# Kernel optimization log

Hardware: AMD Instinct MI355X
Metric: run time of the kernel (lower is better)

The kernel has to match this reference:

```python
import jax, jax.numpy as jnp
import numpy as np

B, S, C = 8, 4096, 1024
H, D, K = 16, 64, 256  # heads, per-head dim, linformer projection dim


def setup_inputs() -> dict:
    key = jax.random.key(0)
    ks = jax.random.split(key, 10)
    sc = 0.02
    return {
        "tensor": jax.random.normal(ks[0], (B, S, C), jnp.float32),
        "to_q_w": jax.random.normal(ks[1], (D, C), jnp.float32) * sc,
        "to_k_w": jax.random.normal(ks[2], (D, C), jnp.float32) * sc,
        "to_v_w": jax.random.normal(ks[3], (D, C), jnp.float32) * sc,
        "wq_w": jax.random.normal(ks[4], (H, D, D), jnp.float32) * sc,
        "wq_b": jnp.zeros((H, D), jnp.float32),
        "wk_w": jax.random.normal(ks[5], (H, D, D), jnp.float32) * sc,
        "wk_b": jnp.zeros((H, D), jnp.float32),
        "wv_w": jax.random.normal(ks[6], (H, D, D), jnp.float32) * sc,
        "wv_b": jnp.zeros((H, D), jnp.float32),
        "E_w": jax.random.normal(ks[7], (K, S), jnp.float32) * sc,
        "E_b": jnp.zeros((K,), jnp.float32),
        "F_w": jax.random.normal(ks[8], (K, S), jnp.float32) * sc,
        "F_b": jnp.zeros((K,), jnp.float32),
        "wo_w": jax.random.normal(ks[9], (C, H * D), jnp.float32) * sc,
        "wo_b": jnp.zeros((C,), jnp.float32),
    }


def reference(tensor, to_q_w, to_k_w, to_v_w, wq_w, wq_b, wk_w, wk_b,
              wv_w, wv_b, E_w, E_b, F_w, F_b, wo_w, wo_b):
    # Shared Q/K/V projections (no bias), recomputed identically per head in torch.
    Q = jnp.einsum('bsc,dc->bsd', tensor, to_q_w)   # [B,S,D]
    Kt = jnp.einsum('bsc,dc->bsd', tensor, to_k_w)
    V = jnp.einsum('bsc,dc->bsd', tensor, to_v_w)

    # Per-head linear layers w_q/w_k/w_v, vectorized over heads.
    QW = jnp.einsum('bsd,hed->bhse', Q, wq_w) + wq_b[None, :, None, :]   # [B,H,S,D]
    KW = jnp.einsum('bsd,hed->bhse', Kt, wk_w) + wk_b[None, :, None, :]  # [B,H,S,D]
    VW = jnp.einsum('bsd,hed->bhse', V, wv_w) + wv_b[None, :, None, :]   # [B,H,S,D]

    # E projection compresses the sequence axis: [B,H,S,D] -> [B,H,D,K]
    KE = jnp.einsum('bhsd,ks->bhdk', KW, E_w) + E_b  # bias broadcasts over last axis K
    # F projection for values, result kept as [B,H,K,D]
    VF = jnp.einsum('bhsd,ks->bhkd', VW, F_w) + F_b[:, None]

    scores = jnp.einsum('bhsd,bhdk->bhsk', QW, KE) / jnp.sqrt(jnp.float32(D))
    P = jax.nn.softmax(scores, axis=-1)              # [B,H,S,K]

    out_h = jnp.einsum('bhsk,bhkd->bhsd', P, VF)     # [B,H,S,D]
    # torch.cat(heads, dim=2): head-major feature layout
    out = out_h.transpose(0, 2, 1, 3).reshape(tensor.shape[0], tensor.shape[1], -1)
    out = jax.nn.gelu(out, approximate=False)        # F.gelu default is exact erf
    out = jnp.einsum('bsf,cf->bsc', out, wo_w) + wo_b
    return out
```

## Files before the change

kernel.cpp:

```cpp
#include <hip/hip_runtime.h>
#include <hip/hip_bf16.h>
#include <math.h>

constexpr int Bn = 8, Sn = 4096, Cn = 1024, Hn = 16, Dn = 64, Kn = 256;
constexpr int BS = Bn * Sn;

typedef __attribute__((ext_vector_type(8))) short bhalf8;
typedef __attribute__((ext_vector_type(4))) float floatx4;
typedef __attribute__((ext_vector_type(4))) unsigned int uix4;

__device__ __forceinline__ float gelu_erf(float x) {
    float z  = x * 0.70710678118654752f;
    float az = fabsf(z);
    float t  = __fdividef(1.0f, fmaf(0.3275911f, az, 1.0f));
    float p  = fmaf(t, 1.061405429f, -1.453152027f);
    p = fmaf(t, p, 1.421413741f);
    p = fmaf(t, p, -0.284496736f);
    p = fmaf(t, p, 0.254829592f);
    p *= t;
    float e  = exp2f(z * z * -1.4426950408889634f);
    float er = copysignf(fmaf(-p, e, 1.0f), z);
    return 0.5f * x * (1.0f + er);
}

__device__ __forceinline__ void gload16(const void* g, void* l) {
    __builtin_amdgcn_global_load_lds(
        (const __attribute__((address_space(1))) unsigned int*)g,
        (__attribute__((address_space(3))) unsigned int*)l,
        16, 0, 0);
}

__global__ __launch_bounds__(256) void k_cast(const float* __restrict__ src, __hip_bfloat16* __restrict__ dst)
{
    int i = (blockIdx.x * 256 + threadIdx.x) * 4;
    float4 v = *reinterpret_cast<const float4*>(src + i);
    union { __hip_bfloat16 h[4]; uint2 u; } pk;
    pk.h[0] = __float2bfloat16(v.x); pk.h[1] = __float2bfloat16(v.y);
    pk.h[2] = __float2bfloat16(v.z); pk.h[3] = __float2bfloat16(v.w);
    *reinterpret_cast<uint2*>(dst + i) = pk.u;
}

__global__ __launch_bounds__(256) void k_qkv(const float* __restrict__ tensor,
    const __hip_bfloat16* __restrict__ Wb,
    __hip_bfloat16* __restrict__ Qb, float* __restrict__ Kp, float* __restrict__ Vp)
{
    __shared__ __align__(16) char Al[64 * 128];
    const int t = threadIdx.x;
    const int w = t >> 6, lane = t & 63, lc = lane & 15, g = lane >> 4;
    const int m0 = blockIdx.x * 64;
    const int wm = (w >> 1) * 32, wn = (w & 1) * 96;
    const int lrow = t >> 2, lq = t & 3;

    floatx4 acc[2][6];
#pragma unroll
    for (int mt = 0; mt < 2; mt++)
#pragma unroll
        for (int nt = 0; nt < 6; nt++) acc[mt][nt] = (floatx4){0.f, 0.f, 0.f, 0.f};

    const float* arow = tensor + (size_t)(m0 + lrow) * 1024;
    float4 f[4];
#pragma unroll
    for (int j = 0; j < 4; j++) f[j] = *reinterpret_cast<const float4*>(arow + (lq + j * 4) * 4);

    for (int kc = 0; kc < 1024; kc += 64) {
        __syncthreads();
#pragma unroll
        for (int j = 0; j < 4; j++) {
            union { __hip_bfloat16 h[4]; uint2 u; } pk;
            pk.h[0] = __float2bfloat16(f[j].x);
            pk.h[1] = __float2bfloat16(f[j].y);
            pk.h[2] = __float2bfloat16(f[j].z);
            pk.h[3] = __float2bfloat16(f[j].w);
            int byt = lrow * 128 + (((lq + j * 4) * 8) ^ ((lrow & 7) << 4));
            *reinterpret_cast<uint2*>(Al + byt) = pk.u;
        }
        __syncthreads();
        int kcn = (kc + 64 < 1024) ? kc + 64 : 0;
#pragma unroll
        for (int j = 0; j < 4; j++) f[j] = *reinterpret_cast<const float4*>(arow + kcn + (lq + j * 4) * 4);
#pragma unroll
        for (int ks = 0; ks < 2; ks++) {
            bhalf8 a[2];
#pragma unroll
            for (int mt = 0; mt < 2; mt++) {
                int row = wm + mt * 16 + lc;
                a[mt] = *reinterpret_cast<const bhalf8*>(Al + row * 128 + ((ks * 64 + g * 16) ^ ((row & 7) << 4)));
            }
#pragma unroll
            for (int nt = 0; nt < 6; nt++) {
                bhalf8 bf = *reinterpret_cast<const bhalf8*>(&Wb[(size_t)(wn + nt * 16 + lc) * 1024 + kc + ks * 32 + g * 8]);
#pragma unroll
                for (int mt = 0; mt < 2; mt++)
                    acc[mt][nt] = __builtin_amdgcn_mfma_f32_16x16x32_bf16(a[mt], bf, acc[mt][nt], 0, 0, 0);
            }
        }
    }
#pragma unroll
    for (int mt = 0; mt < 2; mt++)
#pragma unroll
        for (int nt = 0; nt < 6; nt++) {
            int n = wn + nt * 16 + lc;
#pragma unroll
            for (int i = 0; i < 4; i++) {
                size_t s = (size_t)m0 + wm + mt * 16 + g * 4 + i;
                float v = acc[mt][nt][i];
                if (n < 64)       Qb[s * 64 + n] = __float2bfloat16(v);
                else if (n < 128) Kp[s * 64 + (n - 64)] = v;
                else              Vp[s * 64 + (n - 128)] = v;
            }
        }
}

__global__ __launch_bounds__(256) void k_rowsum(const float* __restrict__ E, const float* __restrict__ F,
                                                float* __restrict__ sumE, float* __restrict__ sumF)
{
    __shared__ float red[256];
    const float* src = blockIdx.y ? F : E;
    float* dst = blockIdx.y ? sumF : sumE;
    const int k = blockIdx.x;
    const int t = threadIdx.x;
    float a = 0.f;
#pragma unroll
    for (int i = 0; i < 16; i++) a += src[(size_t)k * Sn + t + i * 256];
    red[t] = a;
    __syncthreads();
    for (int s = 128; s > 0; s >>= 1) {
        if (t < s) red[t] += red[t + s];
        __syncthreads();
    }
    if (t == 0) dst[k] = red[0];
}

__global__ __launch_bounds__(256) void k_compress(const float* __restrict__ E, const float* __restrict__ F,
    const float* __restrict__ Kp, const float* __restrict__ Vp,
    float* __restrict__ Part)
{
    __shared__ float Es[64 * 33];
    __shared__ float Ps[32 * 64];
    const int zz = blockIdx.z;
    const int mat = zz >> 4, chunk = zz & 15;
    const float* A = mat ? F : E;
    const float* Bm = mat ? Vp : Kp;
    const int b = blockIdx.y;
    const int k0 = blockIdx.x * 64;
    const int sbeg = chunk * 256;
    const int t = threadIdx.x, tx = t & 15, ty = t >> 4;
    float acc[4][4] = {};
    for (int sc = sbeg; sc < sbeg + 256; sc += 32) {
#pragma unroll
        for (int ii = 0; ii < 2; ii++) {
            int idx4 = t + ii * 256;
            int row = idx4 >> 3, col4 = idx4 & 7;
            float4 v = *reinterpret_cast<const float4*>(&A[(size_t)(k0 + row) * Sn + sc + col4 * 4]);
            float* d2 = &Es[row * 33 + col4 * 4];
            d2[0] = v.x; d2[1] = v.y; d2[2] = v.z; d2[3] = v.w;
        }
#pragma unroll
        for (int ii = 0; ii < 2; ii++) {
            int idx4 = t + ii * 256;
            int row = idx4 >> 4, col4 = idx4 & 15;
            float4 v = *reinterpret_cast<const float4*>(&Bm[((size_t)b * Sn + sc + row) * Dn + col4 * 4]);
            float* d2 = &Ps[row * 64 + col4 * 4];
            d2[0] = v.x; d2[1] = v.y; d2[2] = v.z; d2[3] = v.w;
        }
        __syncthreads();
#pragma unroll 8
        for (int kk = 0; kk < 32; kk++) {
            float a[4], w[4];
#pragma unroll
            for (int i = 0; i < 4; i++) a[i] = Es[(ty * 4 + i) * 33 + kk];
#pragma unroll
            for (int j = 0; j < 4; j++) w[j] = Ps[kk * 64 + tx * 4 + j];
#pragma unroll
            for (int i = 0; i < 4; i++)
#pragma unroll
                for (int j = 0; j < 4; j++) acc[i][j] = fmaf(a[i], w[j], acc[i][j]);
        }
        __syncthreads();
    }
    float* pb = Part + (size_t)zz * 131072 + (size_t)b * 16384 + blockIdx.x * 4096;
#pragma unroll
    for (int i = 0; i < 4; i++) {
        float4 v = make_float4(acc[i][0], acc[i][1], acc[i][2], acc[i][3]);
        *reinterpret_cast<float4*>(&pb[(ty * 4 + i) * 64 + tx * 4]) = v;
    }
}

__global__ __launch_bounds__(256) void k_cred(const float* __restrict__ Part,
    __hip_bfloat16* __restrict__ Kc16, __hip_bfloat16* __restrict__ Vc16)
{
    int gid = blockIdx.x * 256 + threadIdx.x;
    int mat = gid >> 17;
    int rem = gid & 131071;
    const float* p = Part + (size_t)mat * 16 * 131072 + rem;
    float s = 0.f;
#pragma unroll
    for (int c = 0; c < 16; c++) s += p[(size_t)c * 131072];
    __hip_bfloat16* dst = mat ? Vc16 : Kc16;
    dst[rem] = __float2bfloat16(s);
}

__global__ __launch_bounds__(256) void k_headw(const float* __restrict__ wq, const float* __restrict__ wqb,
    const float* __restrict__ wk, const float* __restrict__ wkb,
    __hip_bfloat16* __restrict__ Wqk16, float* __restrict__ uArr, float* __restrict__ gArr,
    float* __restrict__ cw, float* __restrict__ cu, float* __restrict__ cg)
{
    __shared__ float wqL[64 * 64], wkL[64 * 64];
    const int h = blockIdx.x, t = threadIdx.x;
#pragma unroll
    for (int ii = 0; ii < 4; ii++) {
        int idx4 = (t + ii * 256) * 4;
        *reinterpret_cast<float4*>(&wqL[idx4]) = *reinterpret_cast<const float4*>(&wq[(size_t)h * 4096 + idx4]);
        *reinterpret_cast<float4*>(&wkL[idx4]) = *reinterpret_cast<const float4*>(&wk[(size_t)h * 4096 + idx4]);
    }
    __syncthreads();
#pragma unroll 2
    for (int ii = 0; ii < 16; ii++) {
        int idx = t + ii * 256;
        int d = idx >> 6, dp = idx & 63;
        float acc = 0.f;
        for (int e = 0; e < 64; e++) acc = fmaf(wqL[e * 64 + d], wkL[e * 64 + dp], acc);
        Wqk16[(size_t)h * 4096 + idx] = __float2bfloat16(acc);
    }
    if (t < 64) {
        int d = t;
        float au = 0.f, ag = 0.f, aw = 0.f;
        for (int e = 0; e < 64; e++) {
            float q = wqL[e * 64 + d];
            au = fmaf(q, wkb[h * 64 + e], au);
            ag += q;
            aw = fmaf(wqb[h * 64 + e], wkL[e * 64 + d], aw);
        }
        uArr[h * 64 + d] = au; gArr[h * 64 + d] = ag; cw[h * 64 + d] = aw;
    }
    if (t == 0) {
        float acu = 0.f, acg = 0.f;
        for (int e = 0; e < 64; e++) {
            acu = fmaf(wqb[h * 64 + e], wkb[h * 64 + e], acu);
            acg += wqb[h * 64 + e];
        }
        cu[h] = acu; cg[h] = acg;
    }
}

__global__ __launch_bounds__(256) void k_proj(
    const __hip_bfloat16* __restrict__ Kc16, const __hip_bfloat16* __restrict__ Vc16,
    const __hip_bfloat16* __restrict__ Wqk16, const __hip_bfloat16* __restrict__ wv16,
    const float* __restrict__ uArr, const float* __restrict__ gArr,
    const float* __restrict__ cw, const float* __restrict__ cu, const float* __restrict__ cg,
    const float* __restrict__ sumE, const float* __restrict__ Eb,
    const float* __restrict__ sumF, const float* __restrict__ Fb,
    const float* __restrict__ wvb,
    __hip_bfloat16* __restrict__ KEqT, __hip_bfloat16* __restrict__ VFT, float* __restrict__ c0)
{
    const int h = blockIdx.x, b = blockIdx.y;
    const int bh = b * Hn + h;
    const int t = threadIdx.x;
    const int w = t >> 6, lane = t & 63, lc = lane & 15, g = lane >> 4;
    const __hip_bfloat16* KcB = Kc16 + (size_t)b * (Kn * 64);
    const __hip_bfloat16* VcB = Vc16 + (size_t)b * (Kn * 64);
    const __hip_bfloat16* Wq = Wqk16 + (size_t)h * 4096;
    const __hip_bfloat16* Wv = wv16 + (size_t)h * 4096;

    {
        floatx4 acc[4][4];
#pragma unroll
        for (int mt = 0; mt < 4; mt++)
#pragma unroll
            for (int nt = 0; nt < 4; nt++) acc[mt][nt] = (floatx4){0.f, 0.f, 0.f, 0.f};
#pragma unroll
        for (int ks = 0; ks < 2; ks++) {
            bhalf8 a[4];
#pragma unroll
            for (int mt = 0; mt < 4; mt++)
                a[mt] = *reinterpret_cast<const bhalf8*>(Wq + (mt * 16 + lc) * 64 + ks * 32 + g * 8);
#pragma unroll
            for (int nt = 0; nt < 4; nt++) {
                bhalf8 bf = *reinterpret_cast<const bhalf8*>(KcB + (size_t)(w * 64 + nt * 16 + lc) * 64 + ks * 32 + g * 8);
#pragma unroll
                for (int mt = 0; mt < 4; mt++)
                    acc[mt][nt] = __builtin_amdgcn_mfma_f32_16x16x32_bf16(a[mt], bf, acc[mt][nt], 0, 0, 0);
            }
        }
#pragma unroll
        for (int mt = 0; mt < 4; mt++) {
            float4 u4 = *reinterpret_cast<const float4*>(&uArr[h * 64 + mt * 16 + g * 4]);
            float4 g4 = *reinterpret_cast<const float4*>(&gArr[h * 64 + mt * 16 + g * 4]);
#pragma unroll
            for (int nt = 0; nt < 4; nt++) {
                int k = w * 64 + nt * 16 + lc;
                float sE = sumE[k], eb = Eb[k];
                union { __hip_bfloat16 hh[4]; uint2 uu; } pk;
                pk.hh[0] = __float2bfloat16(acc[mt][nt][0] + u4.x * sE + g4.x * eb);
                pk.hh[1] = __float2bfloat16(acc[mt][nt][1] + u4.y * sE + g4.y * eb);
                pk.hh[2] = __float2bfloat16(acc[mt][nt][2] + u4.z * sE + g4.z * eb);
                pk.hh[3] = __float2bfloat16(acc[mt][nt][3] + u4.w * sE + g4.w * eb);
                *reinterpret_cast<uint2*>(&KEqT[((size_t)bh * 256 + k) * 64 + mt * 16 + g * 4]) = pk.uu;
            }
        }
    }
    {
        floatx4 acc[4][4];
#pragma unroll
        for (int mt = 0; mt < 4; mt++)
#pragma unroll
            for (int nt = 0; nt < 4; nt++) acc[mt][nt] = (floatx4){0.f, 0.f, 0.f, 0.f};
#pragma unroll
        for (int ks = 0; ks < 2; ks++) {
            bhalf8 a[4];
#pragma unroll
            for (int mt = 0; mt < 4; mt++)
                a[mt] = *reinterpret_cast<const bhalf8*>(VcB + (size_t)(w * 64 + mt * 16 + lc) * 64 + ks * 32 + g * 8);
#pragma unroll
            for (int nt = 0; nt < 4; nt++) {
                bhalf8 bf = *reinterpret_cast<const bhalf8*>(Wv + (nt * 16 + lc) * 64 + ks * 32 + g * 8);
#pragma unroll
                for (int mt = 0; mt < 4; mt++)
                    acc[mt][nt] = __builtin_amdgcn_mfma_f32_16x16x32_bf16(a[mt], bf, acc[mt][nt], 0, 0, 0);
            }
        }
#pragma unroll
        for (int mt = 0; mt < 4; mt++) {
            int kbase = w * 64 + mt * 16 + g * 4;
            float4 sF4 = *reinterpret_cast<const float4*>(&sumF[kbase]);
            float4 fb4 = *reinterpret_cast<const float4*>(&Fb[kbase]);
#pragma unroll
            for (int nt = 0; nt < 4; nt++) {
                int e = nt * 16 + lc;
                float wvbe = wvb[h * 64 + e];
                union { __hip_bfloat16 hh[4]; uint2 uu; } pk;
                pk.hh[0] = __float2bfloat16(acc[mt][nt][0] + wvbe * sF4.x + fb4.x);
                pk.hh[1] = __float2bfloat16(acc[mt][nt][1] + wvbe * sF4.y + fb4.y);
                pk.hh[2] = __float2bfloat16(acc[mt][nt][2] + wvbe * sF4.z + fb4.z);
                pk.hh[3] = __float2bfloat16(acc[mt][nt][3] + wvbe * sF4.w + fb4.w);
                *reinterpret_cast<uint2*>(&VFT[(size_t)bh * 16384 + (size_t)e * 256 + kbase]) = pk.uu;
            }
        }
    }
    {
        constexpr float SC = 0.18033688011112042f;
        const __hip_bfloat16* kr = KcB + (size_t)t * 64;
        float acc = 0.f;
#pragma unroll
        for (int dp = 0; dp < 64; dp++)
            acc = fmaf(cw[h * 64 + dp], __bfloat162float(kr[dp]), acc);
        c0[(size_t)bh * 256 + t] = (acc + cu[h] * sumE[t] + cg[h] * Eb[t]) * SC;
    }
}

__global__ __launch_bounds__(256, 2) void k_attn(
    const __hip_bfloat16* __restrict__ Qb, const __hip_bfloat16* __restrict__ KEqT,
    const float* __restrict__ c0s, const __hip_bfloat16* __restrict__ VFT,
    __hip_bfloat16* __restrict__ cat)
{
    __shared__ __align__(16) char Kl[32768];
    __shared__ __align__(16) char Vl[32768];
    __shared__ __align__(16) char Pl[4 * 2048];
    __shared__ float c0L[256];

    int fid = blockIdx.x + (blockIdx.y << 3);
    int xcd = fid & 7, local = fid >> 3;
    int bh = xcd * 16 + (local & 15);
    int chunk = local >> 4;
    const int b = bh >> 4, h = bh & 15;
    const int t = threadIdx.x;
    const int w = t >> 6, lane = t & 63, lc = lane & 15, g = lane >> 4;

    const char* Kg = reinterpret_cast<const char*>(KEqT + (size_t)bh * 16384);
#pragma unroll
    for (int it = 0; it < 8; ++it) {
        int idx = it * 256 + t;
        int row = idx >> 3, ch = idx & 7;
        gload16(Kg + row * 128 + (ch ^ (row & 7)) * 16, Kl + it * 4096 + w * 1024);
    }
    const char* Vg = reinterpret_cast<const char*>(VFT + (size_t)bh * 16384);
#pragma unroll
    for (int it = 0; it < 8; ++it) {
        int idx = it * 256 + t;
        int row = idx >> 5, c16 = idx & 31;
        gload16(Vg + row * 512 + (c16 ^ (row & 7)) * 16, Vl + it * 4096 + w * 1024);
    }
    c0L[t] = c0s[(size_t)bh * 256 + t];
    __syncthreads();

    char* Pw = Pl + w * 2048;
    const int sbase = chunk * 512 + w * 16;
    constexpr float SC = 0.18033688011112042f;

    const __hip_bfloat16* Q0 = Qb + ((size_t)b * Sn + sbase + lc) * 64 + g * 8;
    bhalf8 bq0 = *reinterpret_cast<const bhalf8*>(Q0);
    bhalf8 bq1 = *reinterpret_cast<const bhalf8*>(Q0 + 32);

    for (int tile = 0; tile < 8; ++tile) {
        asm volatile("" ::: "memory");
        const int s0 = sbase + tile * 64;

        floatx4 acc[16];
#pragma unroll
        for (int rt = 0; rt < 16; rt++) {
            int row = rt * 16 + lc;
            bhalf8 a0 = *reinterpret_cast<const bhalf8*>(Kl + row * 128 + (g ^ (row & 7)) * 16);
            bhalf8 a1 = *reinterpret_cast<const bhalf8*>(Kl + row * 128 + ((4 + g) ^ (row & 7)) * 16);
            floatx4 z = (floatx4){0.f, 0.f, 0.f, 0.f};
            z = __builtin_amdgcn_mfma_f32_16x16x32_bf16(a0, bq0, z, 0, 0, 0);
            z = __builtin_amdgcn_mfma_f32_16x16x32_bf16(a1, bq1, z, 0, 0, 0);
            acc[rt] = z;
        }

        bhalf8 nq0 = bq0, nq1 = bq1;
        if (tile < 7) {
            const __hip_bfloat16* nQ = Qb + ((size_t)b * Sn + s0 + 64 + lc) * 64 + g * 8;
            nq0 = *reinterpret_cast<const bhalf8*>(nQ);
            nq1 = *reinterpret_cast<const bhalf8*>(nQ + 32);
        }

        float ls = 0.f;
#pragma unroll
        for (int rt = 0; rt < 16; rt++) {
            float4 c4 = *reinterpret_cast<const float4*>(&c0L[rt * 16 + g * 4]);
#pragma unroll
            for (int i = 0; i < 4; i++) {
                float e = exp2f(fmaf(acc[rt][i], SC, ((const float*)&c4)[i]));
                acc[rt][i] = e;
                ls += e;
            }
        }
        ls += __shfl_xor(ls, 16);
        ls += __shfl_xor(ls, 32);
        const float linv = 1.f / ls;

        floatx4 o[4];
#pragma unroll
        for (int dt = 0; dt < 4; dt++) o[dt] = (floatx4){0.f, 0.f, 0.f, 0.f};
#pragma unroll
        for (int ph = 0; ph < 4; ++ph) {
#pragma unroll
            for (int rr = 0; rr < 4; rr++) {
                int rt = ph * 4 + rr;
                union { __hip_bfloat16 hh[4]; uint2 u; } pk;
#pragma unroll
                for (int i = 0; i < 4; i++) pk.hh[i] = __float2bfloat16(acc[rt][i]);
                int byt = lc * 128 + ((rr * 32 + g * 8) ^ ((lc & 7) << 4));
                *reinterpret_cast<uint2*>(Pw + byt) = pk.u;
            }
#pragma unroll
            for (int kk = 0; kk < 2; kk++) {
                int ks = ph * 2 + kk;
                bhalf8 pa = *reinterpret_cast<const bhalf8*>(
                    Pw + lc * 128 + ((kk * 64 + g * 16) ^ ((lc & 7) << 4)));
#pragma unroll
                for (int dt = 0; dt < 4; dt++) {
                    int e = dt * 16 + lc;
                    bhalf8 bv = *reinterpret_cast<const bhalf8*>(
                        Vl + e * 512 + (((ks * 4 + g) ^ (e & 7)) * 16));
                    o[dt] = __builtin_amdgcn_mfma_f32_16x16x32_bf16(pa, bv, o[dt], 0, 0, 0);
                }
            }
        }

#pragma unroll
        for (int i = 0; i < 4; i++) {
            float inv_i = __shfl(linv, g * 4 + i);
            int row = g * 4 + i;
#pragma unroll
            for (int dt = 0; dt < 4; dt++) {
                float x = o[dt][i] * inv_i;
                int byt = row * 128 + ((dt * 32 + lc * 2) ^ ((row >> 2) << 5));
                *reinterpret_cast<__hip_bfloat16*>(Pw + byt) = __float2bfloat16(gelu_erf(x));
            }
        }
#pragma unroll
        for (int pass = 0; pass < 2; ++pass) {
            int c = pass * 64 + lane;
            int row = c >> 3, off = (c & 7) * 16;
            uix4 v = *reinterpret_cast<const uix4*>(Pw + row * 128 + (off ^ ((row >> 2) << 5)));
            __hip_bfloat16* dst = cat + ((size_t)b * Sn + s0 + row) * 1024 + h * 64;
            __builtin_nontemporal_store(v, reinterpret_cast<uix4*>(reinterpret_cast<char*>(dst) + off));
        }

        bq0 = nq0; bq1 = nq1;
    }
}

__global__ __launch_bounds__(256, 2) void k_out(
    const __hip_bfloat16* __restrict__ cat, const __hip_bfloat16* __restrict__ wo16,
    const float* __restrict__ wob, float* __restrict__ out)
{
    __shared__ __align__(16) char As[32768];
    __shared__ __align__(16) char Bs[16384];

    const int t = threadIdx.x;
    const int w = t >> 6, lane = t & 63, lc = lane & 15, g = lane >> 4;
    int fid = blockIdx.x + (blockIdx.y << 3);
    int xcd = fid & 7, local = fid >> 3;
    int mt0 = xcd * 16 + (local >> 3);
    int nt0 = local & 7;
    const int m0 = mt0 * 256;
    const int n0 = nt0 * 128;
    const int wm = (w >> 1) * 128, wn = (w & 1) * 64;

    floatx4 acc[8][4];
#pragma unroll
    for (int mt = 0; mt < 8; mt++)
#pragma unroll
        for (int nt = 0; nt < 4; nt++) acc[mt][nt] = (floatx4){0.f, 0.f, 0.f, 0.f};

    for (int kc = 0; kc < 1024; kc += 64) {
        __syncthreads();
#pragma unroll
        for (int call = 0; call < 8; ++call) {
            int idx = call * 256 + t;
            int row = idx >> 3, ch = idx & 7;
            int sch = ch ^ (row & 7);
            gload16(cat + ((size_t)(m0 + row) * 1024 + kc + sch * 8),
                    As + call * 4096 + w * 1024);
        }
#pragma unroll
        for (int call = 0; call < 4; ++call) {
            int idx = call * 256 + t;
            int row = idx >> 3, ch = idx & 7;
            int sch = ch ^ (row & 7);
            gload16(wo16 + ((size_t)(n0 + row) * 1024 + kc + sch * 8),
                    Bs + call * 4096 + w * 1024);
        }
        __syncthreads();

#pragma unroll
        for (int ks = 0; ks < 2; ++ks) {
            bhalf8 a[8], bfr[4];
#pragma unroll
            for (int mt = 0; mt < 8; mt++) {
                int row = wm + mt * 16 + lc;
                int ch = (ks * 4 + g) ^ (row & 7);
                a[mt] = *reinterpret_cast<const bhalf8*>(As + row * 128 + ch * 16);
            }
#pragma unroll
            for (int nt = 0; nt < 4; nt++) {
                int row = wn + nt * 16 + lc;
                int ch = (ks * 4 + g) ^ (row & 7);
                bfr[nt] = *reinterpret_cast<const bhalf8*>(Bs + row * 128 + ch * 16);
            }
#pragma unroll
            for (int mt = 0; mt < 8; mt++)
#pragma unroll
                for (int nt = 0; nt < 4; nt++)
                    acc[mt][nt] = __builtin_amdgcn_mfma_f32_16x16x32_bf16(a[mt], bfr[nt], acc[mt][nt], 0, 0, 0);
        }
    }

#pragma unroll
    for (int mt = 0; mt < 8; mt++)
#pragma unroll
        for (int nt = 0; nt < 4; nt++)
#pragma unroll
            for (int i = 0; i < 4; i++) {
                int row = m0 + wm + mt * 16 + g * 4 + i;
                int col = n0 + wn + nt * 16 + lc;
                __builtin_nontemporal_store(acc[mt][nt][i] + wob[col], &out[(size_t)row * 1024 + col]);
            }
}

extern "C" void kernel_launch(void* const* d_in, const int* in_sizes, int n_in,
                              void* d_out, int out_size, void* d_ws, size_t ws_size,
                              hipStream_t stream) {
    const float* tensor = (const float*)d_in[0];
    const float* to_q   = (const float*)d_in[1];
    const float* to_k   = (const float*)d_in[2];
    const float* to_v   = (const float*)d_in[3];
    const float* wq     = (const float*)d_in[4];
    const float* wqb    = (const float*)d_in[5];
    const float* wk     = (const float*)d_in[6];
    const float* wkb    = (const float*)d_in[7];
    const float* wv     = (const float*)d_in[8];
    const float* wvb    = (const float*)d_in[9];
    const float* Ew     = (const float*)d_in[10];
    const float* Eb     = (const float*)d_in[11];
    const float* Fw     = (const float*)d_in[12];
    const float* Fb     = (const float*)d_in[13];
    const float* wo     = (const float*)d_in[14];
    const float* wob    = (const float*)d_in[15];
    float* out = (float*)d_out;

    float* ws   = (float*)d_ws;
    float* Kp   = ws;
    float* Vp   = Kp + 2097152;
    float* sumE = Vp + 2097152;
    float* sumF = sumE + 256;
    float* uArr = sumF + 256;
    float* gArr = uArr + 1024;
    float* cw   = gArr + 1024;
    float* cu   = cw + 1024;
    float* cg   = cu + 16;
    float* c0   = cg + 16;
    float* fend = c0 + 32768;
    __hip_bfloat16* Qb    = (__hip_bfloat16*)fend;
    __hip_bfloat16* KEqT  = Qb + 2097152;
    __hip_bfloat16* VFT   = KEqT + 2097152;
    __hip_bfloat16* wo16  = VFT + 2097152;
    __hip_bfloat16* Wb    = wo16 + 1048576;
    __hip_bfloat16* Wqk16 = Wb + 196608;
    __hip_bfloat16* wv16  = Wqk16 + 65536;
    __hip_bfloat16* Kc16  = wv16 + 65536;
    __hip_bfloat16* Vc16  = Kc16 + 131072;
    __hip_bfloat16* cat   = Vc16 + 131072;
    float* Part = (float*)cat;

    size_t need = ((char*)(cat + (size_t)BS * 1024)) - (char*)d_ws;
    if (ws_size < need) return;

    k_cast<<<dim3(64),   256, 0, stream>>>(to_q, Wb);
    k_cast<<<dim3(64),   256, 0, stream>>>(to_k, Wb + 65536);
    k_cast<<<dim3(64),   256, 0, stream>>>(to_v, Wb + 131072);
    k_cast<<<dim3(1024), 256, 0, stream>>>(wo, wo16);
    k_cast<<<dim3(64),   256, 0, stream>>>(wv, wv16);

    k_qkv<<<dim3(BS / 64), 256, 0, stream>>>(tensor, Wb, Qb, Kp, Vp);
    k_rowsum<<<dim3(Kn, 2), 256, 0, stream>>>(Ew, Fw, sumE, sumF);
    k_compress<<<dim3(4, Bn, 32), 256, 0, stream>>>(Ew, Fw, Kp, Vp, Part);
    k_cred<<<dim3(1024), 256, 0, stream>>>(Part, Kc16, Vc16);
    k_headw<<<dim3(Hn), 256, 0, stream>>>(wq, wqb, wk, wkb, Wqk16, uArr, gArr, cw, cu, cg);
    k_proj<<<dim3(Hn, Bn), 256, 0, stream>>>(Kc16, Vc16, Wqk16, wv16, uArr, gArr, cw, cu, cg,
                                             sumE, Eb, sumF, Fb, wvb, KEqT, VFT, c0);
    k_attn<<<dim3(8, 128), 256, 0, stream>>>(Qb, KEqT, c0, VFT, cat);
    k_out<<<dim3(Cn / 128, BS / 256), 256, 0, stream>>>(cat, wo16, wob, out);
}
```

Before: 326.4 us.

## Read V from global memory, compute softmax sum via MFMA, raise occupancy

Removes the 32KB V tile from LDS in the attention kernel and reads V fragments directly from global memory (cached) inside the PV loop. The softmax denominator is now taken from an extra MFMA against a vector of ones on the bf16 probabilities, replacing the shuffle reduction. Launch bounds are raised to 3 blocks per SM to exploit the freed LDS. The trade-off is repeated global/L2 loads of V per tile, extra MFMA work, and tighter register limits.

```diff
diff --git a/kernel.cpp b/kernel.cpp
--- a/kernel.cpp
+++ b/kernel.cpp
@@ -348,13 +348,12 @@
     }
 }
 
-__global__ __launch_bounds__(256, 2) void k_attn(
+__global__ __launch_bounds__(256, 3) void k_attn(
     const __hip_bfloat16* __restrict__ Qb, const __hip_bfloat16* __restrict__ KEqT,
     const float* __restrict__ c0s, const __hip_bfloat16* __restrict__ VFT,
     __hip_bfloat16* __restrict__ cat)
 {
     __shared__ __align__(16) char Kl[32768];
-    __shared__ __align__(16) char Vl[32768];
     __shared__ __align__(16) char Pl[4 * 2048];
     __shared__ float c0L[256];
 
@@ -373,19 +372,16 @@
         int row = idx >> 3, ch = idx & 7;
         gload16(Kg + row * 128 + (ch ^ (row & 7)) * 16, Kl + it * 4096 + w * 1024);
     }
-    const char* Vg = reinterpret_cast<const char*>(VFT + (size_t)bh * 16384);
-#pragma unroll
-    for (int it = 0; it < 8; ++it) {
-        int idx = it * 256 + t;
-        int row = idx >> 5, c16 = idx & 31;
-        gload16(Vg + row * 512 + (c16 ^ (row & 7)) * 16, Vl + it * 4096 + w * 1024);
-    }
     c0L[t] = c0s[(size_t)bh * 256 + t];
     __syncthreads();
 
     char* Pw = Pl + w * 2048;
     const int sbase = chunk * 512 + w * 16;
     constexpr float SC = 0.18033688011112042f;
+    const __hip_bfloat16* Vb = VFT + (size_t)bh * 16384;
+
+    const short oneb = (short)0x3F80;
+    const bhalf8 ones = {oneb, oneb, oneb, oneb, oneb, oneb, oneb, oneb};
 
     const __hip_bfloat16* Q0 = Qb + ((size_t)b * Sn + sbase + lc) * 64 + g * 8;
     bhalf8 bq0 = *reinterpret_cast<const bhalf8*>(Q0);
@@ -414,24 +410,18 @@
             nq1 = *reinterpret_cast<const bhalf8*>(nQ + 32);
         }
 
-        float ls = 0.f;
 #pragma unroll
         for (int rt = 0; rt < 16; rt++) {
             float4 c4 = *reinterpret_cast<const float4*>(&c0L[rt * 16 + g * 4]);
 #pragma unroll
-            for (int i = 0; i < 4; i++) {
-                float e = exp2f(fmaf(acc[rt][i], SC, ((const float*)&c4)[i]));
-                acc[rt][i] = e;
-                ls += e;
-            }
-        }
-        ls += __shfl_xor(ls, 16);
-        ls += __shfl_xor(ls, 32);
-        const float linv = 1.f / ls;
-
-        floatx4 o[4];
+            for (int i = 0; i < 4; i++)
+                acc[rt][i] = exp2f(fmaf(acc[rt][i], SC, ((const float*)&c4)[i]));
+        }
+
+        floatx4 o[4], osum;
 #pragma unroll
         for (int dt = 0; dt < 4; dt++) o[dt] = (floatx4){0.f, 0.f, 0.f, 0.f};
+        osum = (floatx4){0.f, 0.f, 0.f, 0.f};
 #pragma unroll
         for (int ph = 0; ph < 4; ++ph) {
 #pragma unroll
@@ -450,17 +440,17 @@
                     Pw + lc * 128 + ((kk * 64 + g * 16) ^ ((lc & 7) << 4)));
 #pragma unroll
                 for (int dt = 0; dt < 4; dt++) {
-                    int e = dt * 16 + lc;
                     bhalf8 bv = *reinterpret_cast<const bhalf8*>(
-                        Vl + e * 512 + (((ks * 4 + g) ^ (e & 7)) * 16));
+                        Vb + (dt * 16 + lc) * 256 + ks * 32 + g * 8);
                     o[dt] = __builtin_amdgcn_mfma_f32_16x16x32_bf16(pa, bv, o[dt], 0, 0, 0);
                 }
+                osum = __builtin_amdgcn_mfma_f32_16x16x32_bf16(pa, ones, osum, 0, 0, 0);
             }
         }
 
 #pragma unroll
         for (int i = 0; i < 4; i++) {
-            float inv_i = __shfl(linv, g * 4 + i);
+            float inv_i = __fdividef(1.f, osum[i]);
             int row = g * 4 + i;
 #pragma unroll
             for (int dt = 0; dt < 4; dt++) {
```

New measurement: 399.8 us. 22.5% more time.
